# Optimization experiments

Measured on AMD Instinct MI355X. Metric: run time of the kernel, lower is better.

The kernel has to match this reference:

```python
import jax, jax.numpy as jnp
import numpy as np

N = 50000   # nodes per graph
E = 1600000 # edges per graph
F = 1024    # literal feature dim (hardcoded in source)
D = 256     # gcn_dims
B = 16384   # ent_ids batch
NUM_HOPS = 3
SLOPE = 0.01  # nn.LeakyReLU default


def spmm(row, col, val, X):
    # sparse [N,N] @ X[N,F] via COO gather + segment-sum
    return jax.ops.segment_sum(val[:, None] * X[col], row, num_segments=N)


def gcn(row, col, val, X, W, b):
    return jax.nn.leaky_relu(spmm(row, col, val, X) @ W + b, SLOPE)


def setup_inputs() -> dict:
    key = jax.random.key(0)
    ks = jax.random.split(key, 24)
    d = {}
    d['ent_lit'] = jax.random.normal(ks[0], (N, F), jnp.float32)
    d['rel_lit'] = jax.random.normal(ks[1], (N, F), jnp.float32)
    d['attr_lit'] = jax.random.normal(ks[2], (N, F), jnp.float32)
    d['ent_val'] = jax.random.uniform(ks[3], (E,), jnp.float32)
    d['rel_val'] = jax.random.uniform(ks[4], (E,), jnp.float32)
    d['attr_val'] = jax.random.uniform(ks[5], (E,), jnp.float32)
    s_in = 1.0 / np.sqrt(F)
    s_d = 1.0 / np.sqrt(D)
    d['W_ent'] = jax.random.normal(ks[6], (F, D), jnp.float32) * s_in
    d['b_ent'] = jnp.zeros((D,), jnp.float32)
    d['W_rel'] = jax.random.normal(ks[7], (F, D), jnp.float32) * s_in
    d['b_rel'] = jnp.zeros((D,), jnp.float32)
    d['W_attr'] = jax.random.normal(ks[8], (F, D), jnp.float32) * s_in
    d['b_attr'] = jnp.zeros((D,), jnp.float32)
    d['W_x'] = jax.random.normal(ks[9], (D, D), jnp.float32) * s_d
    d['b_x'] = jnp.zeros((D,), jnp.float32)
    d['W_lit'] = jax.random.normal(ks[10], (F, D), jnp.float32) * s_in
    d['b_lit'] = jnp.zeros((D,), jnp.float32)
    d['W_gate'] = jax.random.normal(ks[11], (D, D), jnp.float32) * s_d
    d['b_gate'] = jnp.zeros((D,), jnp.float32)
    d['ent_row'] = jax.random.randint(ks[12], (E,), 0, N, jnp.int32)
    d['ent_col'] = jax.random.randint(ks[13], (E,), 0, N, jnp.int32)
    d['rel_row'] = jax.random.randint(ks[14], (E,), 0, N, jnp.int32)
    d['rel_col'] = jax.random.randint(ks[15], (E,), 0, N, jnp.int32)
    d['attr_row'] = jax.random.randint(ks[16], (E,), 0, N, jnp.int32)
    d['attr_col'] = jax.random.randint(ks[17], (E,), 0, N, jnp.int32)
    d['ent_ids'] = jax.random.randint(ks[18], (B,), 0, N, jnp.int32)
    return d


def reference(ent_lit, rel_lit, attr_lit, ent_val, rel_val, attr_val,
              W_ent, b_ent, W_rel, b_rel, W_attr, b_attr, W_x, b_x,
              W_lit, b_lit, W_gate, b_gate,
              ent_row, ent_col, rel_row, rel_col, attr_row, attr_col, ent_ids):
    rel_repr = gcn(rel_row, rel_col, rel_val, rel_lit, W_rel, b_rel)[ent_ids]
    attr_repr = gcn(attr_row, attr_col, attr_val, attr_lit, W_attr, b_attr)[ent_ids]
    ent_literals = ent_lit[ent_ids] @ W_lit + b_lit
    # n-hop gated aggregation
    h = gcn(ent_row, ent_col, ent_val, ent_lit, W_ent, b_ent)
    for _ in range(1, NUM_HOPS):
        nxt = jax.nn.leaky_relu(spmm(ent_row, ent_col, ent_val, h) @ W_x + b_x, SLOPE)
        g = jax.nn.sigmoid(h @ W_gate + b_gate)
        h = g * nxt + (1.0 - g) * h
    ent_n_hop = h[ent_ids]
    return jnp.concatenate([ent_literals, ent_n_hop, rel_repr, attr_repr], axis=1)
```

## Files before the change

kernel.cpp:

```cpp
#include <hip/hip_runtime.h>
#include <math.h>

#define N_NODES 50000
#define N_EDGES 1600000
#define F_DIM 1024
#define D_DIM 256
#define B_IDS 16384

#define BROWS 1024
#define BKT 49
#define NB3 (3 * BKT)
#define CHUNK 4096

typedef __attribute__((ext_vector_type(8))) short bf16x8;
typedef __attribute__((ext_vector_type(4))) float f32x4;

static inline size_t alignup(size_t x) { return (x + 255) & ~(size_t)255; }

__device__ inline unsigned short f2bf(float f) {
  unsigned u = __float_as_uint(f);
  u += 0x7fffu + ((u >> 16) & 1u);
  return (unsigned short)(u >> 16);
}
__device__ inline float bf2f(unsigned short u) {
  return __uint_as_float(((unsigned)u) << 16);
}

__device__ inline void glds16(const void* g, void* l) {
  __builtin_amdgcn_global_load_lds(
      (const __attribute__((address_space(1))) void*)g,
      (__attribute__((address_space(3))) void*)l, 16, 0, 0);
}

struct TrArgs {
  const float* W[6];
  unsigned short* Wh[6];
  unsigned short* Wl[6];
  int K[6];
};

__global__ __launch_bounds__(256) void tr_all_k(TrArgs a) {
  const int z = blockIdx.z;
  const int K = a.K[z];
  if (blockIdx.x * 64 >= K) return;
  const float* W = a.W[z];
  unsigned short* Wt_hi = a.Wh[z];
  unsigned short* Wt_lo = a.Wl[z];
  __shared__ float t[64][65];
  const int k0 = blockIdx.x * 64, n0 = blockIdx.y * 64;
  const int tid = threadIdx.x;
  const int rr = tid >> 4, c4 = (tid & 15) * 4;
#pragma unroll
  for (int q = 0; q < 4; ++q) {
    int row = q * 16 + rr;
    const float4 v = *reinterpret_cast<const float4*>(W + (size_t)(k0 + row) * 256 + n0 + c4);
    t[row][c4 + 0] = v.x; t[row][c4 + 1] = v.y; t[row][c4 + 2] = v.z; t[row][c4 + 3] = v.w;
  }
  __syncthreads();
#pragma unroll
  for (int q = 0; q < 4; ++q) {
    int n = q * 16 + rr;
    ushort4 oh, ol;
    float w0 = t[c4 + 0][n], w1 = t[c4 + 1][n], w2 = t[c4 + 2][n], w3 = t[c4 + 3][n];
    oh.x = f2bf(w0); ol.x = f2bf(w0 - bf2f(oh.x));
    oh.y = f2bf(w1); ol.y = f2bf(w1 - bf2f(oh.y));
    oh.z = f2bf(w2); ol.z = f2bf(w2 - bf2f(oh.z));
    oh.w = f2bf(w3); ol.w = f2bf(w3 - bf2f(oh.w));
    *reinterpret_cast<ushort4*>(Wt_hi + (size_t)(n0 + n) * K + k0 + c4) = oh;
    *reinterpret_cast<ushort4*>(Wt_lo + (size_t)(n0 + n) * K + k0 + c4) = ol;
  }
}


__global__ __launch_bounds__(256) void bcount_k(
    const int* __restrict__ r0, const int* __restrict__ r1, const int* __restrict__ r2,
    int* __restrict__ bcnt)
{
  __shared__ int h[NB3];
  const int t = threadIdx.x;
  for (int i = t; i < NB3; i += 256) h[i] = 0;
  __syncthreads();
  const long long cbase = (long long)blockIdx.x * CHUNK;
  const long long tot = 3LL * N_EDGES;
#pragma unroll
  for (int j = 0; j < 16; ++j) {
    long long idx = cbase + j * 256 + t;
    if (idx < tot) {
      int g = (int)(idx / N_EDGES);
      int e = (int)(idx - (long long)g * N_EDGES);
      int row = (g == 0 ? r0 : g == 1 ? r1 : r2)[e];
      atomicAdd(&h[g * BKT + (row >> 10)], 1);
    }
  }
  __syncthreads();
  for (int i = t; i < NB3; i += 256)
    if (h[i]) atomicAdd(&bcnt[i], h[i]);
}

__global__ void bscan_k(const int* __restrict__ bcnt, int* __restrict__ flatBase,
                        int* __restrict__ cursor) {
  __shared__ int c[NB3];
  const int t = threadIdx.x;
  if (t < NB3) c[t] = bcnt[t];
  __syncthreads();
  if (t < 3) {
    int acc = t * N_EDGES;
    for (int b = 0; b < BKT; ++b) {
      int i = t * BKT + b;
      int v = c[i];
      flatBase[i] = acc;
      cursor[i] = acc;
      acc += v;
    }
  }
  if (t == 0) flatBase[NB3] = 3 * N_EDGES;
}

__global__ __launch_bounds__(256) void bpart_k(
    const int* __restrict__ r0, const int* __restrict__ c0, const float* __restrict__ v0,
    const int* __restrict__ r1, const int* __restrict__ c1, const float* __restrict__ v1,
    const int* __restrict__ r2, const int* __restrict__ c2, const float* __restrict__ v2,
    int* __restrict__ cursor, int2* __restrict__ packed)
{
  __shared__ int hs[256];
  __shared__ int ls[NB3];
  __shared__ int cur[NB3];
  __shared__ int clm[NB3];
  __shared__ int2 stg[CHUNK];
  __shared__ int tgt[CHUNK];
  const int t = threadIdx.x;
  const long long cbase = (long long)blockIdx.x * CHUNK;
  const long long tot = 3LL * N_EDGES;
  hs[t] = 0;
  __syncthreads();
  int rows_[16], gbs_[16];
#pragma unroll
  for (int j = 0; j < 16; ++j) {
    long long idx = cbase + j * 256 + t;
    int gb = -1, row = 0;
    if (idx < tot) {
      int g = (int)(idx / N_EDGES);
      int e = (int)(idx - (long long)g * N_EDGES);
      row = (g == 0 ? r0 : g == 1 ? r1 : r2)[e];
      gb = g * BKT + (row >> 10);
      atomicAdd(&hs[gb], 1);
    }
    gbs_[j] = gb; rows_[j] = row;
  }
  __syncthreads();
  const int myh = hs[t];
  if (t < NB3) clm[t] = atomicAdd(&cursor[t], myh);
  for (int off = 1; off < 256; off <<= 1) {
    int v = (t >= off) ? hs[t - off] : 0;
    __syncthreads();
    hs[t] += v;
    __syncthreads();
  }
  const int excl = hs[t] - myh;
  if (t < NB3) { ls[t] = excl; cur[t] = excl; }
  __syncthreads();
#pragma unroll
  for (int j = 0; j < 16; ++j) {
    const int gb = gbs_[j];
    if (gb >= 0) {
      long long idx = cbase + j * 256 + t;
      int g = (int)(idx / N_EDGES);
      int e = (int)(idx - (long long)g * N_EDGES);
      int col = (g == 0 ? c0 : g == 1 ? c1 : c2)[e];
      float vv = (g == 0 ? v0 : g == 1 ? v1 : v2)[e];
      int slot = atomicAdd(&cur[gb], 1);
      stg[slot] = make_int2(rows_[j] | (col << 16), __float_as_int(vv));
      tgt[slot] = clm[gb] + (slot - ls[gb]);
    }
  }
  __syncthreads();
  const int cnt = (int)min((long long)CHUNK, tot - cbase);
  for (int i = t; i < cnt; i += 256) packed[tgt[i]] = stg[i];
}

__global__ __launch_bounds__(256) void bfinal_k(
    const int2* __restrict__ packed, const int* __restrict__ flatBase,
    int* __restrict__ row_ptr3, int2* __restrict__ cv3)
{
  __shared__ int hist[BROWS];
  __shared__ int part[256];
  const int gb = blockIdx.x;
  const int g = gb / BKT, b = gb % BKT;
  const int rb = b * BROWS;
  const int nrows = min(BROWS, N_NODES - rb);
  const int base = flatBase[gb];
  const int cnt = flatBase[gb + 1] - base;
  const int cvb = base - g * N_EDGES;
  const int t = threadIdx.x;
  for (int i = t; i < BROWS; i += 256) hist[i] = 0;
  __syncthreads();
  for (int i = t; i < cnt; i += 256) {
    int rc = packed[base + i].x;
    atomicAdd(&hist[(rc & 0xffff) - rb], 1);
  }
  __syncthreads();
  const int l0 = hist[4 * t], l1 = hist[4 * t + 1], l2 = hist[4 * t + 2], l3 = hist[4 * t + 3];
  const int s = l0 + l1 + l2 + l3;
  part[t] = s;
  __syncthreads();
  for (int off = 1; off < 256; off <<= 1) {
    int v = (t >= off) ? part[t - off] : 0;
    __syncthreads();
    part[t] += v;
    __syncthreads();
  }
  const int pexcl = part[t] - s;
  const int e0 = pexcl, e1 = e0 + l0, e2 = e1 + l1, e3 = e2 + l2;
  hist[4 * t] = e0; hist[4 * t + 1] = e1; hist[4 * t + 2] = e2; hist[4 * t + 3] = e3;
  int* rp = row_ptr3 + (size_t)g * (N_NODES + 1);
  if (4 * t + 0 < nrows) rp[rb + 4 * t + 0] = cvb + e0;
  if (4 * t + 1 < nrows) rp[rb + 4 * t + 1] = cvb + e1;
  if (4 * t + 2 < nrows) rp[rb + 4 * t + 2] = cvb + e2;
  if (4 * t + 3 < nrows) rp[rb + 4 * t + 3] = cvb + e3;
  if (rb + BROWS >= N_NODES && t == 0) rp[N_NODES] = N_EDGES;
  __syncthreads();
  for (int i = t; i < cnt; i += 256) {
    int2 p = packed[base + i];
    int row = p.x & 0xffff;
    int col = ((unsigned)p.x) >> 16;
    int pos = atomicAdd(&hist[row - rb], 1);
    cv3[base + pos] = make_int2(col, p.y);
  }
}

__global__ void flag_k(const int* __restrict__ ids, unsigned char* __restrict__ flag, int B) {
  int i = blockIdx.x * blockDim.x + threadIdx.x;
  if (i < B) flag[ids[i]] = 1;
}

__global__ __launch_bounds__(256) void spmm_k(
    const int* __restrict__ row_ptr, const int2* __restrict__ cv,
    const unsigned short* __restrict__ srcb, float* __restrict__ dst,
    unsigned short* __restrict__ dstb,
    const float* __restrict__ bias, int do_leaky,
    const unsigned char* __restrict__ flag, int n)
{
  int r = (blockIdx.x << 2) + (threadIdx.x >> 6);
  if (r >= n) return;
  if (flag && !flag[r]) return;
  const int lane = threadIdx.x & 63;
  const int c0 = lane << 2;
  int e0 = row_ptr[r], e1 = row_ptr[r + 1];
  float a0 = 0.f, a1 = 0.f, a2 = 0.f, a3 = 0.f;
  int e = e0;
  for (; e + 3 < e1; e += 4) {
    int2 p0 = cv[e], p1 = cv[e + 1], p2 = cv[e + 2], p3 = cv[e + 3];
    const ushort4 x0 = *reinterpret_cast<const ushort4*>(srcb + (size_t)p0.x * D_DIM + c0);
    const ushort4 x1 = *reinterpret_cast<const ushort4*>(srcb + (size_t)p1.x * D_DIM + c0);
    const ushort4 x2 = *reinterpret_cast<const ushort4*>(srcb + (size_t)p2.x * D_DIM + c0);
    const ushort4 x3 = *reinterpret_cast<const ushort4*>(srcb + (size_t)p3.x * D_DIM + c0);
    const float v0 = __int_as_float(p0.y), v1 = __int_as_float(p1.y);
    const float v2 = __int_as_float(p2.y), v3 = __int_as_float(p3.y);
    a0 = fmaf(v0, bf2f(x0.x), a0); a1 = fmaf(v0, bf2f(x0.y), a1);
    a2 = fmaf(v0, bf2f(x0.z), a2); a3 = fmaf(v0, bf2f(x0.w), a3);
    a0 = fmaf(v1, bf2f(x1.x), a0); a1 = fmaf(v1, bf2f(x1.y), a1);
    a2 = fmaf(v1, bf2f(x1.z), a2); a3 = fmaf(v1, bf2f(x1.w), a3);
    a0 = fmaf(v2, bf2f(x2.x), a0); a1 = fmaf(v2, bf2f(x2.y), a1);
    a2 = fmaf(v2, bf2f(x2.z), a2); a3 = fmaf(v2, bf2f(x2.w), a3);
    a0 = fmaf(v3, bf2f(x3.x), a0); a1 = fmaf(v3, bf2f(x3.y), a1);
    a2 = fmaf(v3, bf2f(x3.z), a2); a3 = fmaf(v3, bf2f(x3.w), a3);
  }
  for (; e < e1; ++e) {
    int2 p = cv[e];
    float v = __int_as_float(p.y);
    const ushort4 x = *reinterpret_cast<const ushort4*>(srcb + (size_t)p.x * D_DIM + c0);
    a0 = fmaf(v, bf2f(x.x), a0); a1 = fmaf(v, bf2f(x.y), a1);
    a2 = fmaf(v, bf2f(x.z), a2); a3 = fmaf(v, bf2f(x.w), a3);
  }
  if (bias) {
    const float4 b = *reinterpret_cast<const float4*>(bias + c0);
    a0 += b.x; a1 += b.y; a2 += b.z; a3 += b.w;
  }
  if (do_leaky) {
    a0 = a0 > 0.f ? a0 : 0.01f * a0;
    a1 = a1 > 0.f ? a1 : 0.01f * a1;
    a2 = a2 > 0.f ? a2 : 0.01f * a2;
    a3 = a3 > 0.f ? a3 : 0.01f * a3;
  }
  *reinterpret_cast<float4*>(dst + (size_t)r * D_DIM + c0) =
      make_float4(a0, a1, a2, a3);
  if (dstb) {
    ushort4 o;
    o.x = f2bf(a0); o.y = f2bf(a1); o.z = f2bf(a2); o.w = f2bf(a3);
    *reinterpret_cast<ushort4*>(dstb + (size_t)r * D_DIM + c0) = o;
  }
}

template<int KT, int MODE>
__global__ __launch_bounds__(256, 4) void mm_k(
    const float* __restrict__ Aptr,
    const unsigned short* __restrict__ Wt_hi,
    const unsigned short* __restrict__ Wt_lo,
    const float* __restrict__ bias,
    float* __restrict__ C, int ldc, int ccol0, int M,
    const int* __restrict__ rowidx,
    const float* __restrict__ nxt, const float* __restrict__ hin,
    unsigned short* __restrict__ Cb)
{
  __shared__ __align__(16) unsigned char smem[32768];
  const int tid = threadIdx.x;
  const int wid = tid >> 6, lane = tid & 63;
  const int wm = wid & 1, wn = wid >> 1;
  const int bm = blockIdx.y * 64;
  const int bn0 = blockIdx.x * 128;
  const int l15 = lane & 15, lk = lane >> 4;

  int mrow[2];
  const float* arow[2];
#pragma unroll
  for (int mi = 0; mi < 2; ++mi) {
    int m = bm + wm * 32 + mi * 16 + l15;
    mrow[mi] = m;
    int sr = (m < M) ? (rowidx ? rowidx[m] : m) : 0;
    arow[mi] = Aptr + (size_t)sr * KT;
  }

  const int st_n = tid >> 2;
  const int st_seg = ((tid & 3) - ((tid >> 3) & 3)) & 3;
  const size_t goA = (size_t)(bn0 + st_n) * KT + st_seg * 8;
  const size_t goB = goA + (size_t)64 * KT;
  const unsigned ldA = tid * 16, ldB = tid * 16 + 4096;

  f32x4 acc[2][4] = {};
  for (int kc = 0; kc < KT / 64; ++kc) {
    const int kk = kc * 64;
    __syncthreads();
    glds16(Wt_hi + goA + kk,      smem + ldA);
    glds16(Wt_hi + goB + kk,      smem + ldB);
    glds16(Wt_hi + goA + kk + 32, smem + 8192 + ldA);
    glds16(Wt_hi + goB + kk + 32, smem + 8192 + ldB);
    glds16(Wt_lo + goA + kk,      smem + 16384 + ldA);
    glds16(Wt_lo + goB + kk,      smem + 16384 + ldB);
    glds16(Wt_lo + goA + kk + 32, smem + 24576 + ldA);
    glds16(Wt_lo + goB + kk + 32, smem + 24576 + ldB);
    bf16x8 ah[2][2], al[2][2];
#pragma unroll
    for (int ks = 0; ks < 2; ++ks) {
      const int ka = kk + ks * 32 + lk * 8;
#pragma unroll
      for (int mi = 0; mi < 2; ++mi) {
        bf16x8 th = {0, 0, 0, 0, 0, 0, 0, 0};
        bf16x8 tl = {0, 0, 0, 0, 0, 0, 0, 0};
        if (mrow[mi] < M) {
          const float* p = arow[mi] + ka;
          const float4 x = *reinterpret_cast<const float4*>(p);
          const float4 y = *reinterpret_cast<const float4*>(p + 4);
#define SPLIT_A(i, val) { unsigned short h_ = f2bf(val); th[i] = (short)h_; \
                          tl[i] = (short)f2bf((val) - bf2f(h_)); }
          SPLIT_A(0, x.x) SPLIT_A(1, x.y) SPLIT_A(2, x.z) SPLIT_A(3, x.w)
          SPLIT_A(4, y.x) SPLIT_A(5, y.y) SPLIT_A(6, y.z) SPLIT_A(7, y.w)
#undef SPLIT_A
        }
        ah[ks][mi] = th; al[ks][mi] = tl;
      }
    }
    __syncthreads();
#pragma unroll
    for (int ks = 0; ks < 2; ++ks) {
#pragma unroll
      for (int f = 0; f < 4; ++f) {
        const int n = wn * 64 + f * 16 + l15;
        const int boff = ks * 8192 + n * 64 + (((lk + (n >> 1)) & 3) << 4);
        const bf16x8 bh = *reinterpret_cast<const bf16x8*>(smem + boff);
        const bf16x8 bl = *reinterpret_cast<const bf16x8*>(smem + 16384 + boff);
#pragma unroll
        for (int mi = 0; mi < 2; ++mi) {
          acc[mi][f] = __builtin_amdgcn_mfma_f32_16x16x32_bf16(ah[ks][mi], bh, acc[mi][f], 0, 0, 0);
          acc[mi][f] = __builtin_amdgcn_mfma_f32_16x16x32_bf16(al[ks][mi], bh, acc[mi][f], 0, 0, 0);
          acc[mi][f] = __builtin_amdgcn_mfma_f32_16x16x32_bf16(ah[ks][mi], bl, acc[mi][f], 0, 0, 0);
        }
      }
    }
  }

  __syncthreads();

#pragma unroll
  for (int mi = 0; mi < 2; ++mi) {
    const int rbase = bm + wm * 32 + mi * 16 + lk * 4;
    int hsrc[4];
    if (MODE == 2) {
#pragma unroll
      for (int r = 0; r < 4; ++r) {
        const int row = rbase + r;
        hsrc[r] = (rowidx && row < M) ? rowidx[row] : row;
      }
    }
#pragma unroll
    for (int f = 0; f < 4; ++f) {
      const int col = bn0 + wn * 64 + f * 16 + l15;
      const float bc = bias ? bias[col] : 0.f;
#pragma unroll
      for (int r = 0; r < 4; ++r) {
        const int row = rbase + r;
        if (row >= M) continue;
        float v = acc[mi][f][r] + bc;
        if (MODE == 1) v = v > 0.f ? v : 0.01f * v;
        if (MODE == 2) {
          const float g = 1.f / (1.f + __expf(-v));
          const float nv = nxt[(size_t)row * D_DIM + col];
          const float hv = hin[(size_t)hsrc[r] * D_DIM + col];
          v = g * nv + (1.f - g) * hv;
        }
        C[(size_t)row * ldc + ccol0 + col] = v;
        if (Cb) Cb[(size_t)row * D_DIM + col] = f2bf(v);
      }
    }
  }
}

template<int KT, int MODE>
__global__ __launch_bounds__(512, 4) void mmw_k(
    const float* __restrict__ Aptr,
    const unsigned short* __restrict__ Wt_hi,
    const unsigned short* __restrict__ Wt_lo,
    const float* __restrict__ bias,
    float* __restrict__ C, int ldc, int ccol0, int M,
    const int* __restrict__ rowidx,
    const float* __restrict__ nxt, const float* __restrict__ hin,
    unsigned short* __restrict__ Cb)
{
  __shared__ __align__(16) unsigned char smem[32768];
  const int tid = threadIdx.x;
  const int wid = tid >> 6, lane = tid & 63;
  const int wm = wid & 3, wn = wid >> 2;
  const int bm = blockIdx.x * 128;
  const int l15 = lane & 15, lk = lane >> 4;

  int mrow[2];
  const float* arow[2];
#pragma unroll
  for (int mi = 0; mi < 2; ++mi) {
    int m = bm + wm * 32 + mi * 16 + l15;
    mrow[mi] = m;
    int sr = (m < M) ? (rowidx ? rowidx[m] : m) : 0;
    arow[mi] = Aptr + (size_t)sr * KT;
  }

  const int s1 = tid, s2 = tid + 512;
  const size_t go1 = (size_t)(s1 >> 2) * KT + ((((s1 & 3) - ((s1 >> 3) & 3)) & 3) << 3);
  const size_t go2 = (size_t)(s2 >> 2) * KT + ((((s2 & 3) - ((s2 >> 3) & 3)) & 3) << 3);

  f32x4 acc[2][8] = {};
  for (int kc = 0; kc < KT / 32; ++kc) {
    const int kk = kc * 32;
    __syncthreads();
    glds16(Wt_hi + go1 + kk, smem + s1 * 16);
    glds16(Wt_hi + go2 + kk, smem + s2 * 16);
    glds16(Wt_lo + go1 + kk, smem + 16384 + s1 * 16);
    glds16(Wt_lo + go2 + kk, smem + 16384 + s2 * 16);
    const int ka = kk + lk * 8;
    bf16x8 ah[2], al[2];
#pragma unroll
    for (int mi = 0; mi < 2; ++mi) {
      bf16x8 th = {0, 0, 0, 0, 0, 0, 0, 0};
      bf16x8 tl = {0, 0, 0, 0, 0, 0, 0, 0};
      if (mrow[mi] < M) {
        const float* p = arow[mi] + ka;
        const float4 x = *reinterpret_cast<const float4*>(p);
        const float4 y = *reinterpret_cast<const float4*>(p + 4);
#define SPLIT_A(i, val) { unsigned short h_ = f2bf(val); th[i] = (short)h_; \
                          tl[i] = (short)f2bf((val) - bf2f(h_)); }
        SPLIT_A(0, x.x) SPLIT_A(1, x.y) SPLIT_A(2, x.z) SPLIT_A(3, x.w)
        SPLIT_A(4, y.x) SPLIT_A(5, y.y) SPLIT_A(6, y.z) SPLIT_A(7, y.w)
#undef SPLIT_A
      }
      ah[mi] = th; al[mi] = tl;
    }
    __syncthreads();
#pragma unroll
    for (int f = 0; f < 8; ++f) {
      const int n = wn * 128 + f * 16 + l15;
      const int boff = n * 64 + (((lk + (n >> 1)) & 3) << 4);
      const bf16x8 bh = *reinterpret_cast<const bf16x8*>(smem + boff);
      const bf16x8 bl = *reinterpret_cast<const bf16x8*>(smem + 16384 + boff);
#pragma unroll
      for (int mi = 0; mi < 2; ++mi) {
        acc[mi][f] = __builtin_amdgcn_mfma_f32_16x16x32_bf16(ah[mi], bh, acc[mi][f], 0, 0, 0);
        acc[mi][f] = __builtin_amdgcn_mfma_f32_16x16x32_bf16(al[mi], bh, acc[mi][f], 0, 0, 0);
        acc[mi][f] = __builtin_amdgcn_mfma_f32_16x16x32_bf16(ah[mi], bl, acc[mi][f], 0, 0, 0);
      }
    }
  }

  __syncthreads();

#pragma unroll
  for (int mi = 0; mi < 2; ++mi) {
    const int rbase = bm + wm * 32 + mi * 16 + lk * 4;
    int hsrc[4];
    if (MODE == 2) {
#pragma unroll
      for (int r = 0; r < 4; ++r) {
        const int row = rbase + r;
        hsrc[r] = (rowidx && row < M) ? rowidx[row] : row;
      }
    }
#pragma unroll
    for (int f = 0; f < 8; ++f) {
      const int col = wn * 128 + f * 16 + l15;
      const float bc = bias ? bias[col] : 0.f;
#pragma unroll
      for (int r = 0; r < 4; ++r) {
        const int row = rbase + r;
        if (row >= M) continue;
        float v = acc[mi][f][r] + bc;
        if (MODE == 1) v = v > 0.f ? v : 0.01f * v;
        if (MODE == 2) {
          const float g = 1.f / (1.f + __expf(-v));
          const float nv = nxt[(size_t)row * D_DIM + col];
          const float hv = hin[(size_t)hsrc[r] * D_DIM + col];
          v = g * nv + (1.f - g) * hv;
        }
        C[(size_t)row * ldc + ccol0 + col] = v;
        if (Cb) Cb[(size_t)row * D_DIM + col] = f2bf(v);
      }
    }
  }
}

__global__ __launch_bounds__(256) void gather_k(const float* __restrict__ src,
                                                const int* __restrict__ ids,
                                                float* __restrict__ dst, int ccol0, int B)
{
  int i = (blockIdx.x << 2) + (threadIdx.x >> 6);
  if (i >= B) return;
  const int lane = threadIdx.x & 63;
  const int c0 = lane << 2;
  const float4 v = *reinterpret_cast<const float4*>(src + (size_t)ids[i] * D_DIM + c0);
  *reinterpret_cast<float4*>(dst + (size_t)i * 1024 + ccol0 + c0) = v;
}

extern "C" void kernel_launch(void* const* d_in, const int* in_sizes, int n_in,
                              void* d_out, int out_size, void* d_ws, size_t ws_size,
                              hipStream_t stream)
{
  const float* ent_lit = (const float*)d_in[0];
  const float* rel_lit = (const float*)d_in[1];
  const float* attr_lit = (const float*)d_in[2];
  const float* ent_val = (const float*)d_in[3];
  const float* rel_val = (const float*)d_in[4];
  const float* attr_val = (const float*)d_in[5];
  const float* W_ent = (const float*)d_in[6];
  const float* b_ent = (const float*)d_in[7];
  const float* W_rel = (const float*)d_in[8];
  const float* b_rel = (const float*)d_in[9];
  const float* W_attr = (const float*)d_in[10];
  const float* b_attr = (const float*)d_in[11];
  const float* W_x = (const float*)d_in[12];
  const float* b_x = (const float*)d_in[13];
  const float* W_lit = (const float*)d_in[14];
  const float* b_lit = (const float*)d_in[15];
  const float* W_gate = (const float*)d_in[16];
  const float* b_gate = (const float*)d_in[17];
  const int* ent_row = (const int*)d_in[18];
  const int* ent_col = (const int*)d_in[19];
  const int* rel_row = (const int*)d_in[20];
  const int* rel_col = (const int*)d_in[21];
  const int* attr_row = (const int*)d_in[22];
  const int* attr_col = (const int*)d_in[23];
  const int* ent_ids = (const int*)d_in[24];
  float* out = (float*)d_out;

  char* p = (char*)d_ws;
  const size_t bufsz = alignup((size_t)N_NODES * D_DIM * 4);
  const size_t bufszb = alignup((size_t)N_NODES * D_DIM * 2);
  const size_t wsz_f = alignup((size_t)F_DIM * D_DIM * 2);
  const size_t wsz_d = alignup((size_t)D_DIM * D_DIM * 2);
  float* B0 = (float*)p; p += bufsz;
  float* B1 = (float*)p; p += bufsz;
  unsigned short* B0b = (unsigned short*)p; p += bufszb;
  unsigned short* B1b = (unsigned short*)p; p += bufszb;
  float* P = (float*)B1b;
  unsigned short* Wh_ent = (unsigned short*)p; p += wsz_f;
  unsigned short* Wl_ent = (unsigned short*)p; p += wsz_f;
  unsigned short* Wh_rel = (unsigned short*)p; p += wsz_f;
  unsigned short* Wl_rel = (unsigned short*)p; p += wsz_f;
  unsigned short* Wh_attr = (unsigned short*)p; p += wsz_f;
  unsigned short* Wl_attr = (unsigned short*)p; p += wsz_f;
  unsigned short* Wh_lit = (unsigned short*)p; p += wsz_f;
  unsigned short* Wl_lit = (unsigned short*)p; p += wsz_f;
  unsigned short* Wh_x = (unsigned short*)p; p += wsz_d;
  unsigned short* Wl_x = (unsigned short*)p; p += wsz_d;
  unsigned short* Wh_gate = (unsigned short*)p; p += wsz_d;
  unsigned short* Wl_gate = (unsigned short*)p; p += wsz_d;
  int* row_ptr3 = (int*)p; p += alignup((size_t)3 * (N_NODES + 1) * 4);
  int* bcnt = (int*)p; p += alignup((size_t)NB3 * 4);
  int* flatBase = (int*)p; p += alignup((size_t)(NB3 + 1) * 4);
  int* cursor = (int*)p; p += alignup((size_t)NB3 * 4);
  unsigned char* flags = (unsigned char*)p; p += alignup((size_t)N_NODES);
  int2* cv3 = (int2*)p; p += alignup((size_t)3 * N_EDGES * 8);
  if ((size_t)(p - (char*)d_ws) > ws_size) return;

  int2* packed = (int2*)B0;

  const int* rp_ent = row_ptr3;
  const int* rp_rel = row_ptr3 + (N_NODES + 1);
  const int* rp_attr = row_ptr3 + 2 * (N_NODES + 1);
  const int2* cv_ent = cv3;
  const int2* cv_rel = cv3 + (size_t)N_EDGES;
  const int2* cv_attr = cv3 + (size_t)2 * N_EDGES;

  dim3 blk(256), blk512(512);
  const int nchunks = (int)((3LL * N_EDGES + CHUNK - 1) / CHUNK);
  dim3 g_spmm((N_NODES + 3) / 4);
  dim3 g_gather((B_IDS + 3) / 4);
  dim3 g_mm_big(2, (N_NODES + 63) / 64);
  dim3 g_mm_ids(2, B_IDS / 64);
  dim3 g_mmw_big((N_NODES + 127) / 128);

  TrArgs ta;
  ta.W[0] = W_ent;  ta.Wh[0] = Wh_ent;  ta.Wl[0] = Wl_ent;  ta.K[0] = F_DIM;
  ta.W[1] = W_rel;  ta.Wh[1] = Wh_rel;  ta.Wl[1] = Wl_rel;  ta.K[1] = F_DIM;
  ta.W[2] = W_attr; ta.Wh[2] = Wh_attr; ta.Wl[2] = Wl_attr; ta.K[2] = F_DIM;
  ta.W[3] = W_lit;  ta.Wh[3] = Wh_lit;  ta.Wl[3] = Wl_lit;  ta.K[3] = F_DIM;
  ta.W[4] = W_x;    ta.Wh[4] = Wh_x;    ta.Wl[4] = Wl_x;    ta.K[4] = D_DIM;
  ta.W[5] = W_gate; ta.Wh[5] = Wh_gate; ta.Wl[5] = Wl_gate; ta.K[5] = D_DIM;
  tr_all_k<<<dim3(F_DIM / 64, 4, 6), blk, 0, stream>>>(ta);

  hipMemsetAsync(bcnt, 0, NB3 * sizeof(int), stream);
  bcount_k<<<dim3(nchunks), blk, 0, stream>>>(ent_row, rel_row, attr_row, bcnt);
  bscan_k<<<dim3(1), blk, 0, stream>>>(bcnt, flatBase, cursor);
  bpart_k<<<dim3(nchunks), blk, 0, stream>>>(ent_row, ent_col, ent_val,
                                             rel_row, rel_col, rel_val,
                                             attr_row, attr_col, attr_val,
                                             cursor, packed);
  bfinal_k<<<dim3(NB3), blk, 0, stream>>>(packed, flatBase, row_ptr3, cv3);

  hipMemsetAsync(flags, 0, N_NODES, stream);
  flag_k<<<dim3(B_IDS / 256), blk, 0, stream>>>(ent_ids, flags, B_IDS);

  mm_k<F_DIM, 0><<<g_mm_big, blk, 0, stream>>>(rel_lit, Wh_rel, Wl_rel, nullptr, B0, D_DIM, 0,
                                               N_NODES, nullptr, nullptr, nullptr, B0b);
  spmm_k<<<g_spmm, blk, 0, stream>>>(rp_rel, cv_rel, B0b, B1, nullptr, b_rel, 1, flags, N_NODES);
  gather_k<<<g_gather, blk, 0, stream>>>(B1, ent_ids, out, 512, B_IDS);

  mm_k<F_DIM, 0><<<g_mm_big, blk, 0, stream>>>(attr_lit, Wh_attr, Wl_attr, nullptr, B0, D_DIM, 0,
                                               N_NODES, nullptr, nullptr, nullptr, B0b);
  spmm_k<<<g_spmm, blk, 0, stream>>>(rp_attr, cv_attr, B0b, B1, nullptr, b_attr, 1, flags, N_NODES);
  gather_k<<<g_gather, blk, 0, stream>>>(B1, ent_ids, out, 768, B_IDS);

  mm_k<F_DIM, 0><<<g_mm_ids, blk, 0, stream>>>(ent_lit, Wh_lit, Wl_lit, b_lit, out, 1024, 0,
                                               B_IDS, ent_ids, nullptr, nullptr, nullptr);

  mm_k<F_DIM, 0><<<g_mm_big, blk, 0, stream>>>(ent_lit, Wh_ent, Wl_ent, nullptr, B0, D_DIM, 0,
                                               N_NODES, nullptr, nullptr, nullptr, B0b);
  spmm_k<<<g_spmm, blk, 0, stream>>>(rp_ent, cv_ent, B0b, B1, B1b, b_ent, 1, nullptr, N_NODES);
  spmm_k<<<g_spmm, blk, 0, stream>>>(rp_ent, cv_ent, B1b, B0, nullptr, nullptr, 0, nullptr, N_NODES);
  mmw_k<D_DIM, 1><<<g_mmw_big, blk512, 0, stream>>>(B0, Wh_x, Wl_x, b_x, B0, D_DIM, 0,
                                                    N_NODES, nullptr, nullptr, nullptr, nullptr);
  mmw_k<D_DIM, 2><<<g_mmw_big, blk512, 0, stream>>>(B1, Wh_gate, Wl_gate, b_gate, B1, D_DIM, 0,
                                                    N_NODES, nullptr, B0, B1, B1b);
  spmm_k<<<g_spmm, blk, 0, stream>>>(rp_ent, cv_ent, B1b, B0, nullptr, nullptr, 0, flags, N_NODES);
  mm_k<D_DIM, 1><<<g_mm_ids, blk, 0, stream>>>(B0, Wh_x, Wl_x, b_x, P, D_DIM, 0,
                                               B_IDS, ent_ids, nullptr, nullptr, nullptr);
  mm_k<D_DIM, 2><<<g_mm_ids, blk, 0, stream>>>(B1, Wh_gate, Wl_gate, b_gate, out, 1024, 256,
                                               B_IDS, ent_ids, P, B1, nullptr);
}
```

Baseline: 1.419 ms.

## Batch three dense projections, two SpMMs and two gathers into grouped launches

Replaces three separate N×1024×256 projection GEMMs with one grouped kernel (blockIdx.y selects graph). It uses 512-thread blocks with 128-row tiles covering all 256 output columns and writes only bf16 output. The rel/attr SpMMs and their gathers are also merged into two-way grouped launches, and a third bf16 buffer is added so the inputs stay live. This cuts launch count, drops the unused fp32 GEMM output writes, and gives each launch more parallel work to fill the GPU. The cost is extra workspace and a heavier per-block register and accumulator footprint in the new GEMM.

```diff
diff --git a/kernel.cpp b/kernel.cpp
--- a/kernel.cpp
+++ b/kernel.cpp
@@ -291,6 +291,151 @@
   }
 }
 
+struct SP2 {
+  const int* rp[2];
+  const int2* cv[2];
+  const unsigned short* src[2];
+  float* dst[2];
+  const float* bias[2];
+};
+__global__ __launch_bounds__(256) void spmm2_k(SP2 a, const unsigned char* __restrict__ flag) {
+  const int z = blockIdx.y;
+  int r = (blockIdx.x << 2) + (threadIdx.x >> 6);
+  if (r >= N_NODES) return;
+  if (!flag[r]) return;
+  const unsigned short* srcb = a.src[z];
+  const int lane = threadIdx.x & 63;
+  const int c0 = lane << 2;
+  int e0 = a.rp[z][r], e1 = a.rp[z][r + 1];
+  const int2* cv = a.cv[z];
+  float a0 = 0.f, a1 = 0.f, a2 = 0.f, a3 = 0.f;
+  int e = e0;
+  for (; e + 3 < e1; e += 4) {
+    int2 p0 = cv[e], p1 = cv[e + 1], p2 = cv[e + 2], p3 = cv[e + 3];
+    const ushort4 x0 = *reinterpret_cast<const ushort4*>(srcb + (size_t)p0.x * D_DIM + c0);
+    const ushort4 x1 = *reinterpret_cast<const ushort4*>(srcb + (size_t)p1.x * D_DIM + c0);
+    const ushort4 x2 = *reinterpret_cast<const ushort4*>(srcb + (size_t)p2.x * D_DIM + c0);
+    const ushort4 x3 = *reinterpret_cast<const ushort4*>(srcb + (size_t)p3.x * D_DIM + c0);
+    const float v0 = __int_as_float(p0.y), v1 = __int_as_float(p1.y);
+    const float v2 = __int_as_float(p2.y), v3 = __int_as_float(p3.y);
+    a0 = fmaf(v0, bf2f(x0.x), a0); a1 = fmaf(v0, bf2f(x0.y), a1);
+    a2 = fmaf(v0, bf2f(x0.z), a2); a3 = fmaf(v0, bf2f(x0.w), a3);
+    a0 = fmaf(v1, bf2f(x1.x), a0); a1 = fmaf(v1, bf2f(x1.y), a1);
+    a2 = fmaf(v1, bf2f(x1.z), a2); a3 = fmaf(v1, bf2f(x1.w), a3);
+    a0 = fmaf(v2, bf2f(x2.x), a0); a1 = fmaf(v2, bf2f(x2.y), a1);
+    a2 = fmaf(v2, bf2f(x2.z), a2); a3 = fmaf(v2, bf2f(x2.w), a3);
+    a0 = fmaf(v3, bf2f(x3.x), a0); a1 = fmaf(v3, bf2f(x3.y), a1);
+    a2 = fmaf(v3, bf2f(x3.z), a2); a3 = fmaf(v3, bf2f(x3.w), a3);
+  }
+  for (; e < e1; ++e) {
+    int2 p = cv[e];
+    float v = __int_as_float(p.y);
+    const ushort4 x = *reinterpret_cast<const ushort4*>(srcb + (size_t)p.x * D_DIM + c0);
+    a0 = fmaf(v, bf2f(x.x), a0); a1 = fmaf(v, bf2f(x.y), a1);
+    a2 = fmaf(v, bf2f(x.z), a2); a3 = fmaf(v, bf2f(x.w), a3);
+  }
+  const float4 b = *reinterpret_cast<const float4*>(a.bias[z] + c0);
+  a0 += b.x; a1 += b.y; a2 += b.z; a3 += b.w;
+  a0 = a0 > 0.f ? a0 : 0.01f * a0;
+  a1 = a1 > 0.f ? a1 : 0.01f * a1;
+  a2 = a2 > 0.f ? a2 : 0.01f * a2;
+  a3 = a3 > 0.f ? a3 : 0.01f * a3;
+  *reinterpret_cast<float4*>(a.dst[z] + (size_t)r * D_DIM + c0) =
+      make_float4(a0, a1, a2, a3);
+}
+
+struct MM3 {
+  const float* A[3];
+  const unsigned short* Wh[3];
+  const unsigned short* Wl[3];
+  unsigned short* Cb[3];
+};
+__global__ __launch_bounds__(512, 4) void mm3_k(MM3 a) {
+  constexpr int KT = F_DIM;
+  const int z = blockIdx.y;
+  const float* __restrict__ Aptr = a.A[z];
+  const unsigned short* __restrict__ Wt_hi = a.Wh[z];
+  const unsigned short* __restrict__ Wt_lo = a.Wl[z];
+  unsigned short* __restrict__ Cb = a.Cb[z];
+
+  __shared__ __align__(16) unsigned char smem[32768];
+  const int tid = threadIdx.x;
+  const int wid = tid >> 6, lane = tid & 63;
+  const int wm = wid & 3, wn = wid >> 2;
+  const int bm = blockIdx.x * 128;
+  const int l15 = lane & 15, lk = lane >> 4;
+
+  int mrow[2];
+  const float* arow[2];
+#pragma unroll
+  for (int mi = 0; mi < 2; ++mi) {
+    int m = bm + wm * 32 + mi * 16 + l15;
+    mrow[mi] = m;
+    arow[mi] = Aptr + (size_t)((m < N_NODES) ? m : 0) * KT;
+  }
+
+  const int s1 = tid, s2 = tid + 512;
+  const size_t go1 = (size_t)(s1 >> 2) * KT + ((((s1 & 3) - ((s1 >> 3) & 3)) & 3) << 3);
+  const size_t go2 = (size_t)(s2 >> 2) * KT + ((((s2 & 3) - ((s2 >> 3) & 3)) & 3) << 3);
+
+  f32x4 acc[2][8] = {};
+  for (int kc = 0; kc < KT / 32; ++kc) {
+    const int kk = kc * 32;
+    __syncthreads();
+    glds16(Wt_hi + go1 + kk, smem + s1 * 16);
+    glds16(Wt_hi + go2 + kk, smem + s2 * 16);
+    glds16(Wt_lo + go1 + kk, smem + 16384 + s1 * 16);
+    glds16(Wt_lo + go2 + kk, smem + 16384 + s2 * 16);
+    const int ka = kk + lk * 8;
+    bf16x8 ah[2], al[2];
+#pragma unroll
+    for (int mi = 0; mi < 2; ++mi) {
+      bf16x8 th = {0, 0, 0, 0, 0, 0, 0, 0};
+      bf16x8 tl = {0, 0, 0, 0, 0, 0, 0, 0};
+      if (mrow[mi] < N_NODES) {
+        const float* p = arow[mi] + ka;
+        const float4 x = *reinterpret_cast<const float4*>(p);
+        const float4 y = *reinterpret_cast<const float4*>(p + 4);
+#define SPLIT_A(i, val) { unsigned short h_ = f2bf(val); th[i] = (short)h_; \
+                          tl[i] = (short)f2bf((val) - bf2f(h_)); }
+        SPLIT_A(0, x.x) SPLIT_A(1, x.y) SPLIT_A(2, x.z) SPLIT_A(3, x.w)
+        SPLIT_A(4, y.x) SPLIT_A(5, y.y) SPLIT_A(6, y.z) SPLIT_A(7, y.w)
+#undef SPLIT_A
+      }
+      ah[mi] = th; al[mi] = tl;
+    }
+    __syncthreads();
+#pragma unroll
+    for (int f = 0; f < 8; ++f) {
+      const int n = wn * 128 + f * 16 + l15;
+      const int boff = n * 64 + (((lk + (n >> 1)) & 3) << 4);
+      const bf16x8 bh = *reinterpret_cast<const bf16x8*>(smem + boff);
+      const bf16x8 bl = *reinterpret_cast<const bf16x8*>(smem + 16384 + boff);
+#pragma unroll
+      for (int mi = 0; mi < 2; ++mi) {
+        acc[mi][f] = __builtin_amdgcn_mfma_f32_16x16x32_bf16(ah[mi], bh, acc[mi][f], 0, 0, 0);
+        acc[mi][f] = __builtin_amdgcn_mfma_f32_16x16x32_bf16(al[mi], bh, acc[mi][f], 0, 0, 0);
+        acc[mi][f] = __builtin_amdgcn_mfma_f32_16x16x32_bf16(ah[mi], bl, acc[mi][f], 0, 0, 0);
+      }
+    }
+  }
+
+#pragma unroll
+  for (int mi = 0; mi < 2; ++mi) {
+    const int rbase = bm + wm * 32 + mi * 16 + lk * 4;
+#pragma unroll
+    for (int f = 0; f < 8; ++f) {
+      const int col = wn * 128 + f * 16 + l15;
+#pragma unroll
+      for (int r = 0; r < 4; ++r) {
+        const int row = rbase + r;
+        if (row >= N_NODES) continue;
+        Cb[(size_t)row * D_DIM + col] = f2bf(acc[mi][f][r]);
+      }
+    }
+  }
+}
+
 template<int KT, int MODE>
 __global__ __launch_bounds__(256, 4) void mm_k(
     const float* __restrict__ Aptr,
@@ -534,6 +679,19 @@
   const int c0 = lane << 2;
   const float4 v = *reinterpret_cast<const float4*>(src + (size_t)ids[i] * D_DIM + c0);
   *reinterpret_cast<float4*>(dst + (size_t)i * 1024 + ccol0 + c0) = v;
+}
+
+struct GA2 { const float* src[2]; int col0[2]; };
+__global__ __launch_bounds__(256) void gather2_k(GA2 a, const int* __restrict__ ids,
+                                                 float* __restrict__ dst)
+{
+  const int z = blockIdx.y;
+  int i = (blockIdx.x << 2) + (threadIdx.x >> 6);
+  if (i >= B_IDS) return;
+  const int lane = threadIdx.x & 63;
+  const int c0 = lane << 2;
+  const float4 v = *reinterpret_cast<const float4*>(a.src[z] + (size_t)ids[i] * D_DIM + c0);
+  *reinterpret_cast<float4*>(dst + (size_t)i * 1024 + a.col0[z] + c0) = v;
 }
 
 extern "C" void kernel_launch(void* const* d_in, const int* in_sizes, int n_in,
@@ -574,9 +732,10 @@
   const size_t wsz_d = alignup((size_t)D_DIM * D_DIM * 2);
   float* B0 = (float*)p; p += bufsz;
   float* B1 = (float*)p; p += bufsz;
-  unsigned short* B0b = (unsigned short*)p; p += bufszb;
-  unsigned short* B1b = (unsigned short*)p; p += bufszb;
-  float* P = (float*)B1b;
+  unsigned short* Bb0 = (unsigned short*)p; p += bufszb;
+  unsigned short* Bb1 = (unsigned short*)p; p += bufszb;
+  unsigned short* Bb2 = (unsigned short*)p; p += bufszb;
+  float* P = (float*)Bb2;
   unsigned short* Wh_ent = (unsigned short*)p; p += wsz_f;
   unsigned short* Wl_ent = (unsigned short*)p; p += wsz_f;
   unsigned short* Wh_rel = (unsigned short*)p; p += wsz_f;
@@ -609,8 +768,10 @@
   dim3 blk(256), blk512(512);
   const int nchunks = (int)((3LL * N_EDGES + CHUNK - 1) / CHUNK);
   dim3 g_spmm((N_NODES + 3) / 4);
+  dim3 g_spmm2((N_NODES + 3) / 4, 2);
   dim3 g_gather((B_IDS + 3) / 4);
-  dim3 g_mm_big(2, (N_NODES + 63) / 64);
+  dim3 g_gather2((B_IDS + 3) / 4, 2);
+  dim3 g_mm3((N_NODES + 127) / 128, 3);
   dim3 g_mm_ids(2, B_IDS / 64);
   dim3 g_mmw_big((N_NODES + 127) / 128);
 
@@ -635,28 +796,32 @@
   hipMemsetAsync(flags, 0, N_NODES, stream);
   flag_k<<<dim3(B_IDS / 256), blk, 0, stream>>>(ent_ids, flags, B_IDS);
 
-  mm_k<F_DIM, 0><<<g_mm_big, blk, 0, stream>>>(rel_lit, Wh_rel, Wl_rel, nullptr, B0, D_DIM, 0,
-                                               N_NODES, nullptr, nullptr, nullptr, B0b);
-  spmm_k<<<g_spmm, blk, 0, stream>>>(rp_rel, cv_rel, B0b, B1, nullptr, b_rel, 1, flags, N_NODES);
-  gather_k<<<g_gather, blk, 0, stream>>>(B1, ent_ids, out, 512, B_IDS);
-
-  mm_k<F_DIM, 0><<<g_mm_big, blk, 0, stream>>>(attr_lit, Wh_attr, Wl_attr, nullptr, B0, D_DIM, 0,
-                                               N_NODES, nullptr, nullptr, nullptr, B0b);
-  spmm_k<<<g_spmm, blk, 0, stream>>>(rp_attr, cv_attr, B0b, B1, nullptr, b_attr, 1, flags, N_NODES);
-  gather_k<<<g_gather, blk, 0, stream>>>(B1, ent_ids, out, 768, B_IDS);
+  MM3 m3;
+  m3.A[0] = rel_lit;  m3.Wh[0] = Wh_rel;  m3.Wl[0] = Wl_rel;  m3.Cb[0] = Bb0;
+  m3.A[1] = attr_lit; m3.Wh[1] = Wh_attr; m3.Wl[1] = Wl_attr; m3.Cb[1] = Bb1;
+  m3.A[2] = ent_lit;  m3.Wh[2] = Wh_ent;  m3.Wl[2] = Wl_ent;  m3.Cb[2] = Bb2;
+  mm3_k<<<g_mm3, blk512, 0, stream>>>(m3);
+
+  SP2 s2;
+  s2.rp[0] = rp_rel;  s2.cv[0] = cv_rel;  s2.src[0] = Bb0; s2.dst[0] = B1; s2.bias[0] = b_rel;
+  s2.rp[1] = rp_attr; s2.cv[1] = cv_attr; s2.src[1] = Bb1; s2.dst[1] = B0; s2.bias[1] = b_attr;
+  spmm2_k<<<g_spmm2, blk, 0, stream>>>(s2, flags);
+
+  GA2 ga;
+  ga.src[0] = B1; ga.col0[0] = 512;
+  ga.src[1] = B0; ga.col0[1] = 768;
+  gather2_k<<<g_gather2, blk, 0, stream>>>(ga, ent_ids, out);
 
   mm_k<F_DIM, 0><<<g_mm_ids, blk, 0, stream>>>(ent_lit, Wh_lit, Wl_lit, b_lit, out, 1024, 0,
                                                B_IDS, ent_ids, nullptr, nullptr, nullptr);
 
-  mm_k<F_DIM, 0><<<g_mm_big, blk, 0, stream>>>(ent_lit, Wh_ent, Wl_ent, nullptr, B0, D_DIM, 0,
-                                               N_NODES, nullptr, nullptr, nullptr, B0b);
-  spmm_k<<<g_spmm, blk, 0, stream>>>(rp_ent, cv_ent, B0b, B1, B1b, b_ent, 1, nullptr, N_NODES);
-  spmm_k<<<g_spmm, blk, 0, stream>>>(rp_ent, cv_ent, B1b, B0, nullptr, nullptr, 0, nullptr, N_NODES);
+  spmm_k<<<g_spmm, blk, 0, stream>>>(rp_ent, cv_ent, Bb2, B1, Bb0, b_ent, 1, nullptr, N_NODES);
+  spmm_k<<<g_spmm, blk, 0, stream>>>(rp_ent, cv_ent, Bb0, B0, nullptr, nullptr, 0, nullptr, N_NODES);
   mmw_k<D_DIM, 1><<<g_mmw_big, blk512, 0, stream>>>(B0, Wh_x, Wl_x, b_x, B0, D_DIM, 0,
                                                     N_NODES, nullptr, nullptr, nullptr, nullptr);
   mmw_k<D_DIM, 2><<<g_mmw_big, blk512, 0, stream>>>(B1, Wh_gate, Wl_gate, b_gate, B1, D_DIM, 0,
-                                                    N_NODES, nullptr, B0, B1, B1b);
-  spmm_k<<<g_spmm, blk, 0, stream>>>(rp_ent, cv_ent, B1b, B0, nullptr, nullptr, 0, flags, N_NODES);
+                                                    N_NODES, nullptr, B0, B1, Bb1);
+  spmm_k<<<g_spmm, blk, 0, stream>>>(rp_ent, cv_ent, Bb1, B0, nullptr, nullptr, 0, flags, N_NODES);
   mm_k<D_DIM, 1><<<g_mm_ids, blk, 0, stream>>>(B0, Wh_x, Wl_x, b_x, P, D_DIM, 0,
                                                B_IDS, ent_ids, nullptr, nullptr, nullptr);
   mm_k<D_DIM, 2><<<g_mm_ids, blk, 0, stream>>>(B1, Wh_gate, Wl_gate, b_gate, out, 1024, 256,
```

After: 1.185 ms. -16.5%, faster.
